# Optimization experiments

Hardware: AMD Instinct MI355X
Metric: run time of the kernel (lower is better)

## Reference

```python
import jax, jax.numpy as jnp
import numpy as np

N_NODES = 100000


def sage_conv(x, src, dst, W_l, W_r, b):
    """PyG-style SAGEConv with mean aggregation:
    out = mean_{j in N(i)} x_j @ W_l + b + x_i @ W_r
    Messages flow edge_index[0] (src) -> edge_index[1] (dst).
    """
    n = x.shape[0]
    msgs = x[src]  # [E, F] gather
    agg = jax.ops.segment_sum(msgs, dst, num_segments=n)  # [N, F]
    cnt = jax.ops.segment_sum(jnp.ones((src.shape[0],), dtype=x.dtype), dst, num_segments=n)
    mean = agg / jnp.clip(cnt, 1.0)[:, None]
    return mean @ W_l + b + x @ W_r


def setup_inputs() -> dict:
    key = jax.random.key(0)
    ks = jax.random.split(key, 12)
    F_in, H, out_c = 128, 128, 1
    E, K = 3200000, 64

    def glorot(k, shape):
        fan_in, fan_out = shape[0], shape[1]
        lim = np.sqrt(6.0 / (fan_in + fan_out))
        return jax.random.uniform(k, shape, jnp.float32, -lim, lim)

    return {
        "x": jax.random.normal(ks[0], (N_NODES, F_in), jnp.float32),
        "edge_index": jax.random.randint(ks[1], (2, E), 0, N_NODES, jnp.int64),
        "curr_idx": 123,
        "dest_idx": 4567,
        "neighbor_indices": jax.random.randint(ks[2], (K,), 0, N_NODES, jnp.int64),
        # conv1 params
        "W1_l": glorot(ks[3], (F_in, H)),
        "W1_r": glorot(ks[4], (F_in, H)),
        "b1": jnp.zeros((H,), jnp.float32),
        # conv2 params
        "W2_l": glorot(ks[5], (H, H)),
        "W2_r": glorot(ks[6], (H, H)),
        "b2": jnp.zeros((H,), jnp.float32),
        # MLP head
        "Wlin1": glorot(ks[7], (3 * H, H)),
        "blin1": jnp.zeros((H,), jnp.float32),
        "Wlin2": glorot(ks[8], (H, out_c)),
        "blin2": jnp.zeros((out_c,), jnp.float32),
    }


def reference(x, edge_index, curr_idx, dest_idx, neighbor_indices,
              W1_l, W1_r, b1, W2_l, W2_r, b2, Wlin1, blin1, Wlin2, blin2):
    src, dst = edge_index[0], edge_index[1]
    h = jax.nn.relu(sage_conv(x, src, dst, W1_l, W1_r, b1))
    node_embs = sage_conv(h, src, dst, W2_l, W2_r, b2)  # [N, H]

    curr_emb = node_embs[curr_idx]  # [H]
    dest_emb = node_embs[dest_idx]  # [H]
    nbr_embs = node_embs[neighbor_indices]  # [K, H]
    K = nbr_embs.shape[0]
    # batched version of the per-neighbor concat + 2-layer MLP
    cat = jnp.concatenate([
        jnp.broadcast_to(curr_emb, (K, curr_emb.shape[0])),
        jnp.broadcast_to(dest_emb, (K, dest_emb.shape[0])),
        nbr_embs,
    ], axis=1)  # [K, 3H]
    hidden = jax.nn.relu(cat @ Wlin1 + blin1)  # [K, H]
    q_values = hidden @ Wlin2 + blin2  # [K, 1]
    return q_values
```

## Files before the change

kernel.cpp:

```cpp
#include <hip/hip_runtime.h>
#include <cstdint>

constexpr int F        = 128;
constexpr int U_CAP    = 8192;
constexpr int T_CAP    = 128;
constexpr int E2_CAP   = 131072;
constexpr int BKT      = 128;
constexpr int BM_WORDS = 3200;
constexpr int SBLK     = 256;
constexpr int EPT      = 32;
constexpr int EPBLK    = SBLK * EPT;
constexpr int LCAP     = 512;


__global__ void k_zero(int* p, int n) {
    int i = blockIdx.x * blockDim.x + threadIdx.x;
    int stride = gridDim.x * blockDim.x;
    for (; i < n; i += stride) p[i] = 0;
}

__global__ void k_build(const int* eidx, int E, int N,
                        const int* curr, const int* dest, const int* nbr, int K,
                        int* hdr, int* t_map, int* u_map,
                        unsigned* t_bm, unsigned* u_bm,
                        int* t_node, int* ent2comp, int* ulist) {
    __shared__ int s_e64, s_n64;
    int tid = threadIdx.x;
    if (tid == 0) { s_e64 = 1; s_n64 = 1; }
    __syncthreads();
    if (tid < 64 && eidx[2 * tid + 1] != 0) s_e64 = 0;
    if (tid < K / 2 && nbr[2 * tid + 1] != 0) s_n64 = 0;
    __syncthreads();
    int n64 = s_n64;
    if (tid == 0) { hdr[4] = s_e64; hdr[5] = s_n64; }

    int node = -1;
    if (tid < K + 2) {
        if (tid == 0)      node = curr[0];
        else if (tid == 1) node = dest[0];
        else               node = n64 ? nbr[2 * (tid - 2)] : nbr[tid - 2];
        if ((unsigned)node < (unsigned)N) {
            if (atomicCAS(&t_map[node], 0, -1) == 0) {
                int slot = atomicAdd(&hdr[0], 1);
                t_node[slot] = node;
                int uid = atomicAdd(&hdr[1], 1);
                ulist[uid] = node;
                atomicExch(&u_map[node], uid + 1);
                if (node < BM_WORDS * 32) {
                    atomicOr(&t_bm[node >> 5], 1u << (node & 31));
                    atomicOr(&u_bm[node >> 5], 1u << (node & 31));
                }
                atomicExch(&t_map[node], slot + 1);
            }
        }
    }
    __syncthreads();
    if (tid < K + 2) {
        int v = ((unsigned)node < (unsigned)N) ? atomicAdd(&t_map[node], 0) : 1;
        ent2comp[tid] = v - 1;
    }
}

static __device__ __forceinline__ int esrc(const int* eidx, int E, int e, int is64) {
    return is64 ? eidx[2 * (size_t)e] : eidx[e];
}
static __device__ __forceinline__ int edst(const int* eidx, int E, int e, int is64) {
    return is64 ? eidx[2 * ((size_t)E + e)] : eidx[(size_t)E + e];
}

__global__ void k_scan1(const int* __restrict__ eidx, int E, int N,
                        const int* __restrict__ t_map, int* u_map,
                        const unsigned* __restrict__ t_bm, unsigned* u_bm,
                        int* hdr, int2* edges2, int* ulist) {
    __shared__ int l_cnt, l_base;
    __shared__ int2 l_buf[LCAP];
    int tid = threadIdx.x;
    if (tid == 0) l_cnt = 0;
    __syncthreads();
    int is64 = hdr[4];
    int be = blockIdx.x * EPBLK;
    int dv[EPT];
    #pragma unroll
    for (int r = 0; r < EPT / 4; ++r) {
        int e0 = be + (r * SBLK + tid) * 4;
        if (!is64 && e0 + 3 < E) {
            int4 d4 = *reinterpret_cast<const int4*>(eidx + (size_t)E + e0);
            dv[r*4+0] = d4.x; dv[r*4+1] = d4.y; dv[r*4+2] = d4.z; dv[r*4+3] = d4.w;
        } else {
            for (int q = 0; q < 4; ++q)
                dv[r*4+q] = (e0 + q < E) ? edst(eidx, E, e0 + q, is64) : -1;
        }
    }
    unsigned wv[EPT];
    #pragma unroll
    for (int i = 0; i < EPT; ++i) {
        int d  = dv[i];
        int dc = ((unsigned)d < (unsigned)N) ? d : 0;
        wv[i] = t_bm[dc >> 5];
    }
    unsigned m = 0;
    #pragma unroll
    for (int i = 0; i < EPT; ++i) {
        int d = dv[i];
        if ((unsigned)d < (unsigned)N && ((wv[i] >> (d & 31)) & 1)) m |= (1u << i);
    }
    while (m) {
        int i = __ffs(m) - 1; m &= m - 1;
        int d = dv[i];
        int tm = t_map[d];
        if (tm <= 0) continue;
        int r = i >> 2, q = i & 3;
        int e = be + (r * SBLK + tid) * 4 + q;
        int s = esrc(eidx, E, e, is64);
        if ((unsigned)s >= (unsigned)N) continue;
        int p = atomicAdd(&l_cnt, 1);
        if (p < LCAP) l_buf[p] = make_int2(s, tm - 1);
        else {
            int gp = atomicAdd(&hdr[2], 1);
            if (gp < E2_CAP) edges2[gp] = make_int2(s, tm - 1);
        }
        if (atomicCAS(&u_map[s], 0, -1) == 0) {
            int id = atomicAdd(&hdr[1], 1);
            if (id < U_CAP) ulist[id] = s;
            if (s < BM_WORDS * 32) atomicOr(&u_bm[s >> 5], 1u << (s & 31));
            __threadfence();
            atomicExch(&u_map[s], id + 1);
        }
    }
    __syncthreads();
    int c = min(l_cnt, LCAP);
    if (c > 0) {
        if (tid == 0) l_base = atomicAdd(&hdr[2], c);
        __syncthreads();
        for (int i = tid; i < c; i += SBLK) {
            int gp = l_base + i;
            if (gp < E2_CAP) edges2[gp] = l_buf[i];
        }
    }
}

__global__ void k_scanU(const int* __restrict__ eidx, int E, int N,
                        const int* __restrict__ u_map,
                        const unsigned* __restrict__ u_bm,
                        const int* __restrict__ hdr,
                        int* deg1, int* bucket) {
    int tid = threadIdx.x;
    int is64 = hdr[4];
    int be = blockIdx.x * EPBLK;
    int dv[EPT];
    #pragma unroll
    for (int r = 0; r < EPT / 4; ++r) {
        int e0 = be + (r * SBLK + tid) * 4;
        if (!is64 && e0 + 3 < E) {
            int4 d4 = *reinterpret_cast<const int4*>(eidx + (size_t)E + e0);
            dv[r*4+0] = d4.x; dv[r*4+1] = d4.y; dv[r*4+2] = d4.z; dv[r*4+3] = d4.w;
        } else {
            for (int q = 0; q < 4; ++q)
                dv[r*4+q] = (e0 + q < E) ? edst(eidx, E, e0 + q, is64) : -1;
        }
    }
    unsigned wv[EPT];
    #pragma unroll
    for (int i = 0; i < EPT; ++i) {
        int d  = dv[i];
        int dc = ((unsigned)d < (unsigned)N) ? d : 0;
        wv[i] = u_bm[dc >> 5];
    }
    unsigned m = 0;
    #pragma unroll
    for (int i = 0; i < EPT; ++i) {
        int d = dv[i];
        if ((unsigned)d < (unsigned)N && ((wv[i] >> (d & 31)) & 1)) m |= (1u << i);
    }
    while (m) {
        int i = __ffs(m) - 1; m &= m - 1;
        int d = dv[i];
        int um = u_map[d];
        if (um <= 0 || um > U_CAP) continue;
        int r = i >> 2, q = i & 3;
        int e = be + (r * SBLK + tid) * 4 + q;
        int s = esrc(eidx, E, e, is64);
        if ((unsigned)s >= (unsigned)N) continue;
        int slot = um - 1;
        int pos = atomicAdd(&deg1[slot], 1);
        if (pos < BKT) bucket[(size_t)slot * BKT + pos] = s;
    }
}

__global__ void k_acc1(const int* __restrict__ deg1, const int* __restrict__ bucket,
                       const int* __restrict__ hdr, int N,
                       const float* __restrict__ x, float* __restrict__ agg1) {
    int b = blockIdx.x;
    if (b >= min(hdr[1], U_CAP)) return;
    int j = threadIdx.x;
    __shared__ int s_src[BKT];
    int dg = deg1[b];
    int stored = min(dg, BKT);
    if (j < stored) s_src[j] = bucket[(size_t)b * BKT + j];
    __syncthreads();
    float acc = 0.0f;
    #pragma unroll 4
    for (int i = 0; i < stored; ++i) {
        int s = s_src[i];
        if ((unsigned)s < (unsigned)N) acc += x[(size_t)s * F + j];
    }
    float c = (dg < 1) ? 1.0f : (float)dg;
    agg1[(size_t)b * F + j] = acc / c;
}

__global__ void k_h(const int* __restrict__ hdr, const int* __restrict__ ulist, int N,
                    const float* __restrict__ agg1,
                    const float* __restrict__ x,
                    const float* __restrict__ W1l, const float* __restrict__ W1r,
                    const float* __restrict__ b1, float* __restrict__ h) {
    int nU = min(hdr[1], U_CAP);
    __shared__ float mean[F];
    __shared__ float xr[F];
    int j = threadIdx.x;
    for (int b = blockIdx.x; b < nU; b += gridDim.x) {
        int node = ulist[b];
        mean[j] = agg1[(size_t)b * F + j];
        xr[j]   = ((unsigned)node < (unsigned)N) ? x[(size_t)node * F + j] : 0.0f;
        __syncthreads();
        float acc = b1[j];
        #pragma unroll 4
        for (int k = 0; k < F; ++k) {
            acc += mean[k] * W1l[k * F + j];
            acc += xr[k]   * W1r[k * F + j];
        }
        h[(size_t)b * F + j] = (acc > 0.0f) ? acc : 0.0f;
        __syncthreads();
    }
}

__global__ void k_acc2(const int2* __restrict__ edges2, const int* __restrict__ hdr, int N,
                       const int* __restrict__ u_map, const float* __restrict__ h,
                       float* agg2, float* cnt2) {
    int nE     = min(hdr[2], E2_CAP);
    int lane   = threadIdx.x & (F - 1);
    int grp    = (blockIdx.x * blockDim.x + threadIdx.x) >> 7;
    int stride = (gridDim.x * blockDim.x) >> 7;
    for (int e = grp; e < nE; e += stride) {
        int2 ed = edges2[e];
        if ((unsigned)ed.x >= (unsigned)N || (unsigned)ed.y >= (unsigned)T_CAP) continue;
        int ui = u_map[ed.x] - 1;
        if ((unsigned)ui >= (unsigned)U_CAP) continue;
        atomicAdd(&agg2[(size_t)ed.y * F + lane], h[(size_t)ui * F + lane]);
        if (lane == 0) atomicAdd(&cnt2[ed.y], 1.0f);
    }
}

__global__ void k_emb(const int* __restrict__ hdr, const int* __restrict__ t_node,
                      const int* __restrict__ u_map, int N,
                      const float* __restrict__ agg2, const float* __restrict__ cnt2,
                      const float* __restrict__ h,
                      const float* __restrict__ W2l, const float* __restrict__ W2r,
                      const float* __restrict__ b2, float* __restrict__ embT) {
    int nT = min(hdr[0], T_CAP);
    int b  = blockIdx.x;
    if (b >= nT) return;
    __shared__ float mean[F];
    __shared__ float hr[F];
    int j    = threadIdx.x;
    int node = t_node[b];
    int ui   = ((unsigned)node < (unsigned)N) ? (u_map[node] - 1) : -1;
    float c  = cnt2[b];
    c = (c < 1.0f) ? 1.0f : c;
    mean[j] = agg2[(size_t)b * F + j] / c;
    hr[j]   = ((unsigned)ui < (unsigned)U_CAP) ? h[(size_t)ui * F + j] : 0.0f;
    __syncthreads();
    float acc = b2[j];
    #pragma unroll 4
    for (int k = 0; k < F; ++k) {
        acc += mean[k] * W2l[k * F + j];
        acc += hr[k]   * W2r[k * F + j];
    }
    embT[(size_t)b * F + j] = acc;
}

__global__ void k_base(const int* __restrict__ ent2comp, const float* __restrict__ embT,
                       const float* __restrict__ Wlin1, const float* __restrict__ blin1,
                       float* __restrict__ base) {
    __shared__ float s_cat[2 * F];
    __shared__ float s_part[4][F];
    int tid = threadIdx.x;
    int g = tid >> 7, j = tid & (F - 1);
    int c0 = ent2comp[0] & (T_CAP - 1);
    int c1 = ent2comp[1] & (T_CAP - 1);
    if (tid < F)          s_cat[tid] = embT[(size_t)c0 * F + tid];
    else if (tid < 2 * F) s_cat[tid] = embT[(size_t)c1 * F + (tid - F)];
    __syncthreads();
    float acc = 0.0f;
    #pragma unroll 4
    for (int i = g * 64; i < (g + 1) * 64; ++i)
        acc += s_cat[i] * Wlin1[i * F + j];
    s_part[g][j] = acc;
    __syncthreads();
    if (g == 0)
        base[j] = blin1[j] + s_part[0][j] + s_part[1][j] + s_part[2][j] + s_part[3][j];
}

static __device__ __forceinline__ float clamp999(int v) {
    return (float)(v < 0 ? 0 : (v > 999 ? 999 : v));
}

__global__ void k_head(const int* __restrict__ hdr, const int* __restrict__ ent2comp,
                       const float* __restrict__ embT,
                       const float* __restrict__ Wlin1, const float* __restrict__ base,
                       const float* __restrict__ Wlin2, const float* __restrict__ blin2,
                       float* __restrict__ out, int K) {
    __shared__ float s_nbr[F];
    __shared__ float s_part[4][F];
    __shared__ float red[F];
    int k = blockIdx.x;
    int tid = threadIdx.x;
    int g = tid >> 7, j = tid & (F - 1);
    int ck = ent2comp[2 + k] & (T_CAP - 1);
    if (tid < F) s_nbr[tid] = embT[(size_t)ck * F + tid];
    __syncthreads();
    const float* W = Wlin1 + 2 * F * F;
    float acc = 0.0f;
    #pragma unroll 4
    for (int i = g * 32; i < (g + 1) * 32; ++i)
        acc += s_nbr[i] * W[i * F + j];
    s_part[g][j] = acc;
    __syncthreads();
    if (g == 0) {
        float hid = base[j] + s_part[0][j] + s_part[1][j] + s_part[2][j] + s_part[3][j];
        hid = (hid > 0.0f) ? hid : 0.0f;
        red[j] = hid * Wlin2[j];
    }
    __syncthreads();
    for (int s = 64; s > 0; s >>= 1) {
        if (tid < s) red[tid] += red[tid + s];
        __syncthreads();
    }
    if (tid == 0) {
        int nT = hdr[0], nU = hdr[1], nE2 = hdr[2];
        float D = 0.0f;
        if      (nT  < 1  || nT  > K + 2)  D = 1.0e6f + clamp999(nT) * 1e3f;
        else if (nU  < nT || nU  > U_CAP)  D = 2.0e6f + clamp999(nU / 10) * 1e3f;
        else if (nE2 < 1  || nE2 > E2_CAP) D = 3.0e6f + clamp999(nE2 / 10) * 1e3f;
        out[k] = red[0] + blin2[0] + D;
    }
}

extern "C" void kernel_launch(void* const* d_in, const int* in_sizes, int n_in,
                              void* d_out, int out_size, void* d_ws, size_t ws_size,
                              hipStream_t stream) {
    const float* x     = (const float*)d_in[0];
    const int*   eidx  = (const int*)d_in[1];
    const int*   curr  = (const int*)d_in[2];
    const int*   dest  = (const int*)d_in[3];
    const int*   nbr   = (const int*)d_in[4];
    const float* W1l   = (const float*)d_in[5];
    const float* W1r   = (const float*)d_in[6];
    const float* b1    = (const float*)d_in[7];
    const float* W2l   = (const float*)d_in[8];
    const float* W2r   = (const float*)d_in[9];
    const float* b2    = (const float*)d_in[10];
    const float* Wlin1 = (const float*)d_in[11];
    const float* blin1 = (const float*)d_in[12];
    const float* Wlin2 = (const float*)d_in[13];
    const float* blin2 = (const float*)d_in[14];
    float* out = (float*)d_out;

    const int N = in_sizes[0] / F;
    const int E = in_sizes[1] / 2;
    const int K = in_sizes[4];

    char*  ws  = (char*)d_ws;
    size_t off = 0;
    int*      hdr      = (int*)(ws + off);      off += 64;
    int*      t_map    = (int*)(ws + off);      off += (size_t)4 * N;
    int*      u_map    = (int*)(ws + off);      off += (size_t)4 * N;
    float*    agg2     = (float*)(ws + off);    off += (size_t)4 * T_CAP * F;
    float*    cnt2     = (float*)(ws + off);    off += (size_t)4 * T_CAP;
    int*      t_node   = (int*)(ws + off);      off += (size_t)4 * T_CAP;
    int*      ent2comp = (int*)(ws + off);      off += (size_t)4 * 256;
    int*      ulist    = (int*)(ws + off);      off += (size_t)4 * U_CAP;
    unsigned* t_bm     = (unsigned*)(ws + off); off += (size_t)4 * BM_WORDS;
    unsigned* u_bm     = (unsigned*)(ws + off); off += (size_t)4 * BM_WORDS;
    int*      deg1     = (int*)(ws + off);      off += (size_t)4 * U_CAP;
    size_t zero_bytes = off;
    int*      bucket   = (int*)(ws + off);      off += (size_t)4 * U_CAP * BKT;
    float*    agg1     = (float*)(ws + off);    off += (size_t)4 * U_CAP * F;
    int2*     edges2   = (int2*)(ws + off);     off += (size_t)8 * E2_CAP;
    float*    h        = (float*)(ws + off);    off += (size_t)4 * U_CAP * F;
    float*    embT     = (float*)(ws + off);    off += (size_t)4 * T_CAP * F;
    float*    base     = (float*)(ws + off);    off += (size_t)4 * F;

    int zero_words = (int)(zero_bytes / 4);
    k_zero<<<1024, 256, 0, stream>>>((int*)d_ws, zero_words);

    k_build<<<1, 128, 0, stream>>>(eidx, E, N, curr, dest, nbr, K, hdr, t_map, u_map,
                                   t_bm, u_bm, t_node, ent2comp, ulist);

    int sg = (E + EPBLK - 1) / EPBLK;
    k_scan1<<<sg, SBLK, 0, stream>>>(eidx, E, N, t_map, u_map, t_bm, u_bm,
                                     hdr, edges2, ulist);
    k_scanU<<<sg, SBLK, 0, stream>>>(eidx, E, N, u_map, u_bm, hdr, deg1, bucket);
    k_acc1<<<U_CAP, 128, 0, stream>>>(deg1, bucket, hdr, N, x, agg1);
    k_h<<<2048, 128, 0, stream>>>(hdr, ulist, N, agg1, x, W1l, W1r, b1, h);
    k_acc2<<<256, 256, 0, stream>>>(edges2, hdr, N, u_map, h, agg2, cnt2);
    k_emb<<<K + 2, 128, 0, stream>>>(hdr, t_node, u_map, N, agg2, cnt2, h, W2l, W2r, b2, embT);
    k_base<<<1, 512, 0, stream>>>(ent2comp, embT, Wlin1, blin1, base);
    k_head<<<K, 512, 0, stream>>>(hdr, ent2comp, embT, Wlin1, base, Wlin2, blin2, out, K);
}
```

Before: 251.3 us.

## Fuse layer-1 aggregation with transform, scan layer-2 edges per target, merge head kernels

Doubles edges per thread in the two edge-scan kernels and uses a 64-bit hit mask, folding the bitmap load into the mask loop. It fuses layer-1 neighbor mean aggregation into the per-node linear transform, so the agg1 buffer goes away. Layer-2 aggregation now has each target block scan the compact edge list, replacing global float atomics. The base and head MLP kernels are merged. This cuts kernel launches, intermediate traffic and atomics, at the cost of redundant edge-list scans per target, fewer blocks for layer 1 (256 instead of 8192), and recomputing the shared concat product in every head block.

```diff
diff --git a/kernel.cpp b/kernel.cpp
--- a/kernel.cpp
+++ b/kernel.cpp
@@ -8,7 +8,7 @@
 constexpr int BKT      = 128;
 constexpr int BM_WORDS = 3200;
 constexpr int SBLK     = 256;
-constexpr int EPT      = 32;
+constexpr int EPT      = 64;
 constexpr int EPBLK    = SBLK * EPT;
 constexpr int LCAP     = 512;
 
@@ -91,21 +91,17 @@
                 dv[r*4+q] = (e0 + q < E) ? edst(eidx, E, e0 + q, is64) : -1;
         }
     }
-    unsigned wv[EPT];
+    unsigned long long m = 0;
     #pragma unroll
     for (int i = 0; i < EPT; ++i) {
         int d  = dv[i];
         int dc = ((unsigned)d < (unsigned)N) ? d : 0;
-        wv[i] = t_bm[dc >> 5];
-    }
-    unsigned m = 0;
-    #pragma unroll
-    for (int i = 0; i < EPT; ++i) {
-        int d = dv[i];
-        if ((unsigned)d < (unsigned)N && ((wv[i] >> (d & 31)) & 1)) m |= (1u << i);
+        unsigned w = t_bm[dc >> 5];
+        if ((unsigned)d < (unsigned)N && ((w >> (d & 31)) & 1))
+            m |= (1ull << i);
     }
     while (m) {
-        int i = __ffs(m) - 1; m &= m - 1;
+        int i = __ffsll(m) - 1; m &= m - 1;
         int d = dv[i];
         int tm = t_map[d];
         if (tm <= 0) continue;
@@ -159,21 +155,17 @@
                 dv[r*4+q] = (e0 + q < E) ? edst(eidx, E, e0 + q, is64) : -1;
         }
     }
-    unsigned wv[EPT];
+    unsigned long long m = 0;
     #pragma unroll
     for (int i = 0; i < EPT; ++i) {
         int d  = dv[i];
         int dc = ((unsigned)d < (unsigned)N) ? d : 0;
-        wv[i] = u_bm[dc >> 5];
-    }
-    unsigned m = 0;
-    #pragma unroll
-    for (int i = 0; i < EPT; ++i) {
-        int d = dv[i];
-        if ((unsigned)d < (unsigned)N && ((wv[i] >> (d & 31)) & 1)) m |= (1u << i);
+        unsigned w = u_bm[dc >> 5];
+        if ((unsigned)d < (unsigned)N && ((w >> (d & 31)) & 1))
+            m |= (1ull << i);
     }
     while (m) {
-        int i = __ffs(m) - 1; m &= m - 1;
+        int i = __ffsll(m) - 1; m &= m - 1;
         int d = dv[i];
         int um = u_map[d];
         if (um <= 0 || um > U_CAP) continue;
@@ -187,87 +179,79 @@
     }
 }
 
-__global__ void k_acc1(const int* __restrict__ deg1, const int* __restrict__ bucket,
-                       const int* __restrict__ hdr, int N,
-                       const float* __restrict__ x, float* __restrict__ agg1) {
-    int b = blockIdx.x;
-    if (b >= min(hdr[1], U_CAP)) return;
-    int j = threadIdx.x;
+__global__ void k_l1(const int* __restrict__ deg1, const int* __restrict__ bucket,
+                     const int* __restrict__ hdr, const int* __restrict__ ulist, int N,
+                     const float* __restrict__ x,
+                     const float* __restrict__ W1l, const float* __restrict__ W1r,
+                     const float* __restrict__ b1, float* __restrict__ h) {
+    int nU = min(hdr[1], U_CAP);
     __shared__ int s_src[BKT];
-    int dg = deg1[b];
-    int stored = min(dg, BKT);
-    if (j < stored) s_src[j] = bucket[(size_t)b * BKT + j];
-    __syncthreads();
-    float acc = 0.0f;
-    #pragma unroll 4
-    for (int i = 0; i < stored; ++i) {
-        int s = s_src[i];
-        if ((unsigned)s < (unsigned)N) acc += x[(size_t)s * F + j];
-    }
-    float c = (dg < 1) ? 1.0f : (float)dg;
-    agg1[(size_t)b * F + j] = acc / c;
-}
-
-__global__ void k_h(const int* __restrict__ hdr, const int* __restrict__ ulist, int N,
-                    const float* __restrict__ agg1,
-                    const float* __restrict__ x,
-                    const float* __restrict__ W1l, const float* __restrict__ W1r,
-                    const float* __restrict__ b1, float* __restrict__ h) {
-    int nU = min(hdr[1], U_CAP);
     __shared__ float mean[F];
     __shared__ float xr[F];
     int j = threadIdx.x;
     for (int b = blockIdx.x; b < nU; b += gridDim.x) {
+        int dg = deg1[b];
+        int stored = min(dg, BKT);
+        if (j < stored) s_src[j] = bucket[(size_t)b * BKT + j];
         int node = ulist[b];
-        mean[j] = agg1[(size_t)b * F + j];
-        xr[j]   = ((unsigned)node < (unsigned)N) ? x[(size_t)node * F + j] : 0.0f;
-        __syncthreads();
-        float acc = b1[j];
+        xr[j] = ((unsigned)node < (unsigned)N) ? x[(size_t)node * F + j] : 0.0f;
+        __syncthreads();
+        float acc = 0.0f;
+        #pragma unroll 4
+        for (int i = 0; i < stored; ++i) {
+            int s = s_src[i];
+            if ((unsigned)s < (unsigned)N) acc += x[(size_t)s * F + j];
+        }
+        float c = (dg < 1) ? 1.0f : (float)dg;
+        mean[j] = acc / c;
+        __syncthreads();
+        float o = b1[j];
         #pragma unroll 4
         for (int k = 0; k < F; ++k) {
-            acc += mean[k] * W1l[k * F + j];
-            acc += xr[k]   * W1r[k * F + j];
-        }
-        h[(size_t)b * F + j] = (acc > 0.0f) ? acc : 0.0f;
-        __syncthreads();
-    }
-}
-
-__global__ void k_acc2(const int2* __restrict__ edges2, const int* __restrict__ hdr, int N,
-                       const int* __restrict__ u_map, const float* __restrict__ h,
-                       float* agg2, float* cnt2) {
-    int nE     = min(hdr[2], E2_CAP);
-    int lane   = threadIdx.x & (F - 1);
-    int grp    = (blockIdx.x * blockDim.x + threadIdx.x) >> 7;
-    int stride = (gridDim.x * blockDim.x) >> 7;
-    for (int e = grp; e < nE; e += stride) {
-        int2 ed = edges2[e];
-        if ((unsigned)ed.x >= (unsigned)N || (unsigned)ed.y >= (unsigned)T_CAP) continue;
-        int ui = u_map[ed.x] - 1;
-        if ((unsigned)ui >= (unsigned)U_CAP) continue;
-        atomicAdd(&agg2[(size_t)ed.y * F + lane], h[(size_t)ui * F + lane]);
-        if (lane == 0) atomicAdd(&cnt2[ed.y], 1.0f);
-    }
-}
-
-__global__ void k_emb(const int* __restrict__ hdr, const int* __restrict__ t_node,
-                      const int* __restrict__ u_map, int N,
-                      const float* __restrict__ agg2, const float* __restrict__ cnt2,
-                      const float* __restrict__ h,
-                      const float* __restrict__ W2l, const float* __restrict__ W2r,
-                      const float* __restrict__ b2, float* __restrict__ embT) {
+            o += mean[k] * W1l[k * F + j];
+            o += xr[k]   * W1r[k * F + j];
+        }
+        h[(size_t)b * F + j] = (o > 0.0f) ? o : 0.0f;
+        __syncthreads();
+    }
+}
+
+__global__ void k_l2(const int* __restrict__ hdr, const int* __restrict__ t_node,
+                     const int* __restrict__ u_map, int N,
+                     const int2* __restrict__ edges2, const float* __restrict__ h,
+                     const float* __restrict__ W2l, const float* __restrict__ W2r,
+                     const float* __restrict__ b2, float* __restrict__ embT) {
     int nT = min(hdr[0], T_CAP);
     int b  = blockIdx.x;
     if (b >= nT) return;
+    int nE2 = min(hdr[2], E2_CAP);
+    __shared__ int s_ui[256];
+    __shared__ int s_cnt;
     __shared__ float mean[F];
     __shared__ float hr[F];
-    int j    = threadIdx.x;
+    int j = threadIdx.x;
+    if (j == 0) s_cnt = 0;
+    __syncthreads();
+    for (int i = j; i < nE2; i += 128) {
+        int2 ed = edges2[i];
+        if (ed.y == b) {
+            int ui = ((unsigned)ed.x < (unsigned)N) ? (u_map[ed.x] - 1) : -1;
+            if ((unsigned)ui < (unsigned)U_CAP) {
+                int p = atomicAdd(&s_cnt, 1);
+                if (p < 256) s_ui[p] = ui;
+            }
+        }
+    }
+    __syncthreads();
+    int cnt = min(s_cnt, 256);
+    float sum = 0.0f;
+    #pragma unroll 4
+    for (int i = 0; i < cnt; ++i) sum += h[(size_t)s_ui[i] * F + j];
+    float c = (s_cnt < 1) ? 1.0f : (float)s_cnt;
+    mean[j] = sum / c;
     int node = t_node[b];
-    int ui   = ((unsigned)node < (unsigned)N) ? (u_map[node] - 1) : -1;
-    float c  = cnt2[b];
-    c = (c < 1.0f) ? 1.0f : c;
-    mean[j] = agg2[(size_t)b * F + j] / c;
-    hr[j]   = ((unsigned)ui < (unsigned)U_CAP) ? h[(size_t)ui * F + j] : 0.0f;
+    int ui = ((unsigned)node < (unsigned)N) ? (u_map[node] - 1) : -1;
+    hr[j] = ((unsigned)ui < (unsigned)U_CAP) ? h[(size_t)ui * F + j] : 0.0f;
     __syncthreads();
     float acc = b2[j];
     #pragma unroll 4
@@ -278,55 +262,36 @@
     embT[(size_t)b * F + j] = acc;
 }
 
-__global__ void k_base(const int* __restrict__ ent2comp, const float* __restrict__ embT,
-                       const float* __restrict__ Wlin1, const float* __restrict__ blin1,
-                       float* __restrict__ base) {
-    __shared__ float s_cat[2 * F];
-    __shared__ float s_part[4][F];
-    int tid = threadIdx.x;
-    int g = tid >> 7, j = tid & (F - 1);
-    int c0 = ent2comp[0] & (T_CAP - 1);
-    int c1 = ent2comp[1] & (T_CAP - 1);
-    if (tid < F)          s_cat[tid] = embT[(size_t)c0 * F + tid];
-    else if (tid < 2 * F) s_cat[tid] = embT[(size_t)c1 * F + (tid - F)];
-    __syncthreads();
-    float acc = 0.0f;
-    #pragma unroll 4
-    for (int i = g * 64; i < (g + 1) * 64; ++i)
-        acc += s_cat[i] * Wlin1[i * F + j];
-    s_part[g][j] = acc;
-    __syncthreads();
-    if (g == 0)
-        base[j] = blin1[j] + s_part[0][j] + s_part[1][j] + s_part[2][j] + s_part[3][j];
-}
-
 static __device__ __forceinline__ float clamp999(int v) {
     return (float)(v < 0 ? 0 : (v > 999 ? 999 : v));
 }
 
-__global__ void k_head(const int* __restrict__ hdr, const int* __restrict__ ent2comp,
-                       const float* __restrict__ embT,
-                       const float* __restrict__ Wlin1, const float* __restrict__ base,
-                       const float* __restrict__ Wlin2, const float* __restrict__ blin2,
-                       float* __restrict__ out, int K) {
-    __shared__ float s_nbr[F];
+__global__ void k_headf(const int* __restrict__ hdr, const int* __restrict__ ent2comp,
+                        const float* __restrict__ embT,
+                        const float* __restrict__ Wlin1, const float* __restrict__ blin1,
+                        const float* __restrict__ Wlin2, const float* __restrict__ blin2,
+                        float* __restrict__ out, int K) {
+    __shared__ float s_cat[3 * F];
     __shared__ float s_part[4][F];
     __shared__ float red[F];
     int k = blockIdx.x;
     int tid = threadIdx.x;
     int g = tid >> 7, j = tid & (F - 1);
+    int c0 = ent2comp[0] & (T_CAP - 1);
+    int c1 = ent2comp[1] & (T_CAP - 1);
     int ck = ent2comp[2 + k] & (T_CAP - 1);
-    if (tid < F) s_nbr[tid] = embT[(size_t)ck * F + tid];
-    __syncthreads();
-    const float* W = Wlin1 + 2 * F * F;
+    if (tid < F)          s_cat[tid] = embT[(size_t)c0 * F + tid];
+    else if (tid < 2 * F) s_cat[tid] = embT[(size_t)c1 * F + (tid - F)];
+    else if (tid < 3 * F) s_cat[tid] = embT[(size_t)ck * F + (tid - 2 * F)];
+    __syncthreads();
     float acc = 0.0f;
     #pragma unroll 4
-    for (int i = g * 32; i < (g + 1) * 32; ++i)
-        acc += s_nbr[i] * W[i * F + j];
+    for (int i = g * 96; i < (g + 1) * 96; ++i)
+        acc += s_cat[i] * Wlin1[i * F + j];
     s_part[g][j] = acc;
     __syncthreads();
     if (g == 0) {
-        float hid = base[j] + s_part[0][j] + s_part[1][j] + s_part[2][j] + s_part[3][j];
+        float hid = blin1[j] + s_part[0][j] + s_part[1][j] + s_part[2][j] + s_part[3][j];
         hid = (hid > 0.0f) ? hid : 0.0f;
         red[j] = hid * Wlin2[j];
     }
@@ -374,8 +339,6 @@
     int*      hdr      = (int*)(ws + off);      off += 64;
     int*      t_map    = (int*)(ws + off);      off += (size_t)4 * N;
     int*      u_map    = (int*)(ws + off);      off += (size_t)4 * N;
-    float*    agg2     = (float*)(ws + off);    off += (size_t)4 * T_CAP * F;
-    float*    cnt2     = (float*)(ws + off);    off += (size_t)4 * T_CAP;
     int*      t_node   = (int*)(ws + off);      off += (size_t)4 * T_CAP;
     int*      ent2comp = (int*)(ws + off);      off += (size_t)4 * 256;
     int*      ulist    = (int*)(ws + off);      off += (size_t)4 * U_CAP;
@@ -384,11 +347,9 @@
     int*      deg1     = (int*)(ws + off);      off += (size_t)4 * U_CAP;
     size_t zero_bytes = off;
     int*      bucket   = (int*)(ws + off);      off += (size_t)4 * U_CAP * BKT;
-    float*    agg1     = (float*)(ws + off);    off += (size_t)4 * U_CAP * F;
     int2*     edges2   = (int2*)(ws + off);     off += (size_t)8 * E2_CAP;
     float*    h        = (float*)(ws + off);    off += (size_t)4 * U_CAP * F;
     float*    embT     = (float*)(ws + off);    off += (size_t)4 * T_CAP * F;
-    float*    base     = (float*)(ws + off);    off += (size_t)4 * F;
 
     int zero_words = (int)(zero_bytes / 4);
     k_zero<<<1024, 256, 0, stream>>>((int*)d_ws, zero_words);
@@ -400,10 +361,7 @@
     k_scan1<<<sg, SBLK, 0, stream>>>(eidx, E, N, t_map, u_map, t_bm, u_bm,
                                      hdr, edges2, ulist);
     k_scanU<<<sg, SBLK, 0, stream>>>(eidx, E, N, u_map, u_bm, hdr, deg1, bucket);
-    k_acc1<<<U_CAP, 128, 0, stream>>>(deg1, bucket, hdr, N, x, agg1);
-    k_h<<<2048, 128, 0, stream>>>(hdr, ulist, N, agg1, x, W1l, W1r, b1, h);
-    k_acc2<<<256, 256, 0, stream>>>(edges2, hdr, N, u_map, h, agg2, cnt2);
-    k_emb<<<K + 2, 128, 0, stream>>>(hdr, t_node, u_map, N, agg2, cnt2, h, W2l, W2r, b2, embT);
-    k_base<<<1, 512, 0, stream>>>(ent2comp, embT, Wlin1, blin1, base);
-    k_head<<<K, 512, 0, stream>>>(hdr, ent2comp, embT, Wlin1, base, Wlin2, blin2, out, K);
-}
+    k_l1<<<256, 128, 0, stream>>>(deg1, bucket, hdr, ulist, N, x, W1l, W1r, b1, h);
+    k_l2<<<T_CAP, 128, 0, stream>>>(hdr, t_node, u_map, N, edges2, h, W2l, W2r, b2, embT);
+    k_headf<<<K, 512, 0, stream>>>(hdr, ent2comp, embT, Wlin1, blin1, Wlin2, blin2, out, K);
+}
```

New measurement: 374.3 us. +49.0%, slower.
